# Performance work log

Hardware: AMD Instinct MI355X
Metric: run time of the kernel (lower is better)

Reference implementation:

```python
import jax, jax.numpy as jnp
import numpy as np

E = 1024      # embed_dim (== embed_dim_)
NH = 8        # num_heads
HD = E // NH  # head_dim
BS1 = 2048
BS2 = 2048
EPS = 1e-5


def _layernorm(x, g, b):
    m = jnp.mean(x, axis=-1, keepdims=True)
    v = jnp.mean(jnp.square(x - m), axis=-1, keepdims=True)
    return (x - m) * jax.lax.rsqrt(v + EPS) * g + b


def setup_inputs() -> dict:
    key = jax.random.key(0)
    ks = jax.random.split(key, 16)
    s = 1.0 / np.sqrt(E)
    s4 = 1.0 / np.sqrt(4 * E)
    inp = {
        "x1": jax.random.normal(ks[0], (BS1, E), jnp.float32),
        "x2": jax.random.normal(ks[1], (BS2, E), jnp.float32),
        "Wq": jax.random.uniform(ks[2], (E, E), jnp.float32, -s, s),
        "bq": jax.random.uniform(ks[3], (E,), jnp.float32, -s, s),
        "Wk": jax.random.uniform(ks[4], (E, E), jnp.float32, -s, s),
        "bk": jax.random.uniform(ks[5], (E,), jnp.float32, -s, s),
        "Wv": jax.random.uniform(ks[6], (E, E), jnp.float32, -s, s),
        "bv": jax.random.uniform(ks[7], (E,), jnp.float32, -s, s),
        "Wo": jax.random.uniform(ks[8], (E, E), jnp.float32, -s, s),
        "bo": jax.random.uniform(ks[9], (E,), jnp.float32, -s, s),
        "W1": jax.random.uniform(ks[10], (4 * E, E), jnp.float32, -s, s),
        "b1": jax.random.uniform(ks[11], (4 * E,), jnp.float32, -s, s),
        "W2": jax.random.uniform(ks[12], (E, 4 * E), jnp.float32, -s4, s4),
        "b2": jax.random.uniform(ks[13], (E,), jnp.float32, -s4, s4),
        "g1": jnp.ones((E,), jnp.float32),
        "be1": jnp.zeros((E,), jnp.float32),
        "g2": jnp.ones((E,), jnp.float32),
        "be2": jnp.zeros((E,), jnp.float32),
    }
    return inp


def reference(x1, x2, Wq, bq, Wk, bk, Wv, bv, Wo, bo, W1, b1, W2, b2, g1, be1, g2, be2):
    scale = HD ** -0.5
    # Projections; attention runs over the batch axis (n=bs1, m=bs2)
    q = (x1 @ Wq.T + bq).reshape(BS1, NH, HD)   # [n,h,d]
    k = (x2 @ Wk.T + bk).reshape(BS2, NH, HD)   # [m,h,d]
    v = (x2 @ Wv.T + bv).reshape(BS2, NH, HD)   # [m,h,d]
    scores = jnp.einsum('nhd,mhd->nmh', q, k) * scale  # [n,m,h]
    # NOTE: faithful to source: softmax over the HEADS axis (dim=-1)
    probs = jax.nn.softmax(scores, axis=-1)
    # dropout is identity in eval mode
    attn = jnp.einsum('nmh,mhd->nhd', probs, v).reshape(BS1, E)
    attn = attn @ Wo.T + bo
    h = _layernorm(x1 + attn, g1, be1)
    ffn = jax.nn.relu(h @ W1.T + b1) @ W2.T + b2
    return _layernorm(h + ffn, g2, be2)
```

## Files before the change

kernel.cpp:

```cpp
#include <hip/hip_runtime.h>

#define BS 2048
#define EMB 1024
#define NHEAD 8
#define HDIM 128

typedef unsigned short u16;
typedef __attribute__((ext_vector_type(8))) short bf16x8;
typedef __attribute__((ext_vector_type(4))) float f32x4;

__device__ __forceinline__ u16 f32_bf16(float f) {
  unsigned u = __float_as_uint(f);
  u += 0x7fffu + ((u >> 16) & 1u);
  return (u16)(u >> 16);
}
__device__ __forceinline__ float bf2f(u16 x) {
  return __uint_as_float((unsigned)x << 16);
}

__device__ __forceinline__ void gld_lds16(const void* g, void* l) {
  __builtin_amdgcn_global_load_lds(
      (const __attribute__((address_space(1))) void*)g,
      (__attribute__((address_space(3))) void*)l, 16, 0, 0);
}

struct CvtArgs { const float* src[8]; };
__global__ __launch_bounds__(256) void cvt_all(CvtArgs a, u16* __restrict__ dst) {
  long i = (long)blockIdx.x * 256 + threadIdx.x;
  int seg = (int)(i >> 18);
  const float* src; long b;
  if (seg < 2)       { src = a.src[0]; b = 0; }
  else if (seg < 4)  { src = a.src[1]; b = 2L << 18; }
  else if (seg == 4) { src = a.src[2]; b = 4L << 18; }
  else if (seg == 5) { src = a.src[3]; b = 5L << 18; }
  else if (seg == 6) { src = a.src[4]; b = 6L << 18; }
  else if (seg == 7) { src = a.src[5]; b = 7L << 18; }
  else if (seg < 12) { src = a.src[6]; b = 8L << 18; }
  else               { src = a.src[7]; b = 12L << 18; }
  float4 v = ((const float4*)src)[i - b];
  ushort4 o;
  o.x = f32_bf16(v.x); o.y = f32_bf16(v.y); o.z = f32_bf16(v.z); o.w = f32_bf16(v.w);
  ((ushort4*)dst)[i] = o;
}

__device__ __forceinline__ void gemm_core(
    const u16* __restrict__ A, const u16* __restrict__ B, void* __restrict__ Cp,
    const float* __restrict__ bias, int K, int lda, int ldb, int ldc,
    long cbase, int mode, int relu, int m0, int n0) {
  __shared__ __align__(16) u16 As[128 * 32];
  __shared__ __align__(16) u16 Bs[128 * 32];
  const int t = threadIdx.x;
  const int lane = t & 63, l15 = lane & 15, quad = lane >> 4;
  const int wv = t >> 6, wr = wv & 1, wc = wv >> 1;
  const int wbase = t & ~63;

  f32x4 acc[4][4];
#pragma unroll
  for (int r = 0; r < 4; ++r)
#pragma unroll
    for (int c = 0; c < 4; ++c) acc[r][c] = (f32x4){0.f, 0.f, 0.f, 0.f};

  for (int k0 = 0; k0 < K; k0 += 32) {
#pragma unroll
    for (int i = 0; i < 2; ++i) {
      int s = i * 256 + t;
      gld_lds16(A + (long)(m0 + (s >> 2)) * lda + k0 + (s & 3) * 8,
                As + (i * 256 + wbase) * 8);
    }
#pragma unroll
    for (int i = 0; i < 2; ++i) {
      int s = i * 256 + t;
      gld_lds16(B + (long)(n0 + (s >> 2)) * ldb + k0 + (s & 3) * 8,
                Bs + (i * 256 + wbase) * 8);
    }
    __syncthreads();
    bf16x8 fa[4], fb[4];
#pragma unroll
    for (int r = 0; r < 4; ++r)
      fa[r] = *(const bf16x8*)&As[(wr * 64 + r * 16 + l15) * 32 + quad * 8];
#pragma unroll
    for (int c = 0; c < 4; ++c)
      fb[c] = *(const bf16x8*)&Bs[(wc * 64 + c * 16 + l15) * 32 + quad * 8];
#pragma unroll
    for (int r = 0; r < 4; ++r)
#pragma unroll
      for (int c = 0; c < 4; ++c)
        acc[r][c] = __builtin_amdgcn_mfma_f32_16x16x32_bf16(fa[r], fb[c], acc[r][c], 0, 0, 0);
    __syncthreads();
  }

#pragma unroll
  for (int r = 0; r < 4; ++r)
#pragma unroll
    for (int c = 0; c < 4; ++c) {
      const int m = m0 + wr * 64 + r * 16 + quad * 4;
      const int n = n0 + wc * 64 + c * 16 + l15;
      const float bv = bias ? bias[n] : 0.f;
      f32x4 v = acc[r][c];
      if (mode == 2) {
        ushort4 o;
        o.x = f32_bf16(v[0] + bv);
        o.y = f32_bf16(v[1] + bv);
        o.z = f32_bf16(v[2] + bv);
        o.w = f32_bf16(v[3] + bv);
        *(ushort4*)((u16*)Cp + cbase + (long)n * ldc + m) = o;
      } else {
#pragma unroll
        for (int i = 0; i < 4; ++i) {
          float x = v[i] + bv;
          if (relu) x = fmaxf(x, 0.f);
          if (mode == 0)
            ((float*)Cp)[cbase + (long)(m + i) * ldc + n] = x;
          else
            ((u16*)Cp)[cbase + (long)(m + i) * ldc + n] = f32_bf16(x);
        }
      }
    }
}

__global__ __launch_bounds__(256) void gemm_bt_k(
    const u16* __restrict__ A, const u16* __restrict__ B, void* __restrict__ C,
    const float* __restrict__ bias, int K, int lda, int ldb, int ldc,
    long aOffZ, long bOffZ, long cOffZ, int mode, int relu) {
  gemm_core(A + (long)blockIdx.z * aOffZ, B + (long)blockIdx.z * bOffZ, C, bias,
            K, lda, ldb, ldc, (long)blockIdx.z * cOffZ, mode, relu,
            blockIdx.y * 128, blockIdx.x * 128);
}

__global__ __launch_bounds__(256) void qkv_kernel(
    const u16* __restrict__ x1b, const u16* __restrict__ x2b,
    const u16* __restrict__ Wqb, const u16* __restrict__ Wkb, const u16* __restrict__ Wvb,
    const float* __restrict__ bq, const float* __restrict__ bk, const float* __restrict__ bv,
    u16* __restrict__ Qb, u16* __restrict__ Kb, u16* __restrict__ Vt) {
  const int z = blockIdx.z;
  const u16* A = (z == 0) ? x1b : x2b;
  const u16* B = (z == 0) ? Wqb : (z == 1) ? Wkb : Wvb;
  void* C = (z == 0) ? (void*)Qb : (z == 1) ? (void*)Kb : (void*)Vt;
  const float* bias = (z == 0) ? bq : (z == 1) ? bk : bv;
  const int mode = (z == 2) ? 2 : 1;
  const int ldc = (z == 2) ? 2048 : 1024;
  gemm_core(A, B, C, bias, 1024, 1024, 1024, ldc, 0, mode, 0,
            blockIdx.y * 128, blockIdx.x * 128);
}

__global__ __launch_bounds__(256) void pv_kernel(
    const u16* __restrict__ P, const u16* __restrict__ Vt, u16* __restrict__ parts) {
  const int h = blockIdx.z >> 1, ks = blockIdx.z & 1;
  const u16* A = P + (long)h * BS * BS + ks * 1024;
  const u16* B = Vt + (long)h * HDIM * 2048 + ks * 1024;
  const long cbase = (long)ks * BS * 1024 + h * HDIM;
  gemm_core(A, B, parts, nullptr, 1024, 2048, 2048, 1024, cbase, 1, 0,
            blockIdx.y * 128, 0);
}

__global__ __launch_bounds__(256) void reduce2_bf16(
    const u16* __restrict__ p0, const u16* __restrict__ p1, u16* __restrict__ out) {
  int i = blockIdx.x * 256 + threadIdx.x;
  ushort4 a = ((const ushort4*)p0)[i];
  ushort4 b = ((const ushort4*)p1)[i];
  ushort4 o;
  o.x = f32_bf16(bf2f(a.x) + bf2f(b.x));
  o.y = f32_bf16(bf2f(a.y) + bf2f(b.y));
  o.z = f32_bf16(bf2f(a.z) + bf2f(b.z));
  o.w = f32_bf16(bf2f(a.w) + bf2f(b.w));
  ((ushort4*)out)[i] = o;
}

__global__ __launch_bounds__(256) void scores_softmax(
    const u16* __restrict__ Q, const u16* __restrict__ Km, u16* __restrict__ P) {
  __shared__ __align__(16) u16 Qs[32 * 128];
  __shared__ __align__(16) u16 Ks[128 * 128];
  const int t = threadIdx.x;
  const int lane = t & 63, l15 = lane & 15, quad = lane >> 4;
  const int wv = t >> 6;
  const int n0 = blockIdx.y * 32, m0 = blockIdx.x * 128;
  const int wbase = t & ~63;

  f32x4 acc[8][2][2];
#pragma unroll
  for (int h = 0; h < 8; ++h)
#pragma unroll
    for (int r = 0; r < 2; ++r)
#pragma unroll
      for (int c = 0; c < 2; ++c) acc[h][r][c] = (f32x4){0.f, 0.f, 0.f, 0.f};

#pragma unroll
  for (int h = 0; h < 8; ++h) {
#pragma unroll
    for (int i = 0; i < 2; ++i) {
      int s = i * 256 + t;
      gld_lds16(Q + (long)(n0 + ((s >> 2) & 31)) * EMB + h * HDIM + (s >> 7) * 32 + (s & 3) * 8,
                Qs + (i * 256 + wbase) * 8);
    }
#pragma unroll
    for (int i = 0; i < 8; ++i) {
      int s = i * 256 + t;
      gld_lds16(Km + (long)(m0 + ((s >> 2) & 127)) * EMB + h * HDIM + (s >> 9) * 32 + (s & 3) * 8,
                Ks + (i * 256 + wbase) * 8);
    }
    __syncthreads();
#pragma unroll
    for (int kk = 0; kk < 4; ++kk) {
      bf16x8 fa[2], fb[2];
#pragma unroll
      for (int r = 0; r < 2; ++r)
        fa[r] = *(const bf16x8*)&Qs[kk * 1024 + (r * 16 + l15) * 32 + quad * 8];
#pragma unroll
      for (int c = 0; c < 2; ++c)
        fb[c] = *(const bf16x8*)&Ks[kk * 4096 + (wv * 32 + c * 16 + l15) * 32 + quad * 8];
#pragma unroll
      for (int r = 0; r < 2; ++r)
#pragma unroll
        for (int c = 0; c < 2; ++c)
          acc[h][r][c] = __builtin_amdgcn_mfma_f32_16x16x32_bf16(fa[r], fb[c], acc[h][r][c], 0, 0, 0);
    }
    __syncthreads();
  }

  const float scale = 0.08838834764831845f;
#pragma unroll
  for (int r = 0; r < 2; ++r)
#pragma unroll
    for (int c = 0; c < 2; ++c)
#pragma unroll
      for (int i = 0; i < 4; ++i) {
        float mx = acc[0][r][c][i];
#pragma unroll
        for (int h = 1; h < 8; ++h) mx = fmaxf(mx, acc[h][r][c][i]);
        float sum = 0.f;
#pragma unroll
        for (int h = 0; h < 8; ++h) {
          float e = __expf((acc[h][r][c][i] - mx) * scale);
          acc[h][r][c][i] = e;
          sum += e;
        }
        float inv = 1.f / sum;
#pragma unroll
        for (int h = 0; h < 8; ++h) acc[h][r][c][i] *= inv;
      }

#pragma unroll
  for (int h = 0; h < 8; ++h) {
#pragma unroll
    for (int r = 0; r < 2; ++r)
#pragma unroll
      for (int c = 0; c < 2; ++c)
#pragma unroll
        for (int i = 0; i < 4; ++i) {
          int nl = r * 16 + quad * 4 + i;
          int ml = (wv * 32 + c * 16 + l15) ^ (quad << 3);
          Qs[nl * 128 + ml] = f32_bf16(acc[h][r][c][i]);
        }
    __syncthreads();
#pragma unroll
    for (int j = 0; j < 2; ++j) {
      int ch = j * 256 + t;
      int row = ch >> 4;
      int col = (ch & 15) * 8;
      int sw = ((row >> 2) & 3) << 3;
      uint4 val = *(const uint4*)&Qs[row * 128 + (col ^ sw)];
      *(uint4*)&P[(long)h * BS * BS + (long)(n0 + row) * BS + m0 + col] = val;
    }
    __syncthreads();
  }
}

__global__ __launch_bounds__(256) void ln_residual3(
    const float* __restrict__ x, const float* __restrict__ y0, const float* __restrict__ y1,
    const float* __restrict__ colb, const float* __restrict__ g, const float* __restrict__ b,
    float* __restrict__ out32, u16* __restrict__ out16) {
  const int row = blockIdx.x, t = threadIdx.x;
  float4 v = ((const float4*)(x + (long)row * EMB))[t];
  float4 u0 = ((const float4*)(y0 + (long)row * EMB))[t];
  float4 u1 = ((const float4*)(y1 + (long)row * EMB))[t];
  float4 cb = ((const float4*)colb)[t];
  v.x += u0.x + u1.x + cb.x;
  v.y += u0.y + u1.y + cb.y;
  v.z += u0.z + u1.z + cb.z;
  v.w += u0.w + u1.w + cb.w;
  float s = v.x + v.y + v.z + v.w;
  float q = v.x * v.x + v.y * v.y + v.z * v.z + v.w * v.w;
#pragma unroll
  for (int off = 32; off > 0; off >>= 1) {
    s += __shfl_xor(s, off);
    q += __shfl_xor(q, off);
  }
  __shared__ float red[8];
  const int wv = t >> 6, lane = t & 63;
  if (lane == 0) { red[wv] = s; red[4 + wv] = q; }
  __syncthreads();
  s = red[0] + red[1] + red[2] + red[3];
  q = red[4] + red[5] + red[6] + red[7];
  const float mean = s * (1.f / EMB);
  const float var = q * (1.f / EMB) - mean * mean;
  const float rstd = rsqrtf(var + 1e-5f);
  float4 gg = ((const float4*)g)[t];
  float4 bb = ((const float4*)b)[t];
  float4 o;
  o.x = (v.x - mean) * rstd * gg.x + bb.x;
  o.y = (v.y - mean) * rstd * gg.y + bb.y;
  o.z = (v.z - mean) * rstd * gg.z + bb.z;
  o.w = (v.w - mean) * rstd * gg.w + bb.w;
  ((float4*)(out32 + (long)row * EMB))[t] = o;
  if (out16) {
    ushort4 ho;
    ho.x = f32_bf16(o.x); ho.y = f32_bf16(o.y); ho.z = f32_bf16(o.z); ho.w = f32_bf16(o.w);
    ((ushort4*)(out16 + (long)row * EMB))[t] = ho;
  }
}

extern "C" void kernel_launch(void* const* d_in, const int* in_sizes, int n_in,
                              void* d_out, int out_size, void* d_ws, size_t ws_size,
                              hipStream_t stream) {
  const float* x1 = (const float*)d_in[0];
  const float* x2 = (const float*)d_in[1];
  const float* Wq = (const float*)d_in[2];
  const float* bq = (const float*)d_in[3];
  const float* Wk = (const float*)d_in[4];
  const float* bk = (const float*)d_in[5];
  const float* Wv = (const float*)d_in[6];
  const float* bv = (const float*)d_in[7];
  const float* Wo = (const float*)d_in[8];
  const float* bo = (const float*)d_in[9];
  const float* W1 = (const float*)d_in[10];
  const float* b1 = (const float*)d_in[11];
  const float* W2 = (const float*)d_in[12];
  const float* b2 = (const float*)d_in[13];
  const float* g1 = (const float*)d_in[14];
  const float* be1 = (const float*)d_in[15];
  const float* g2 = (const float*)d_in[16];
  const float* be2 = (const float*)d_in[17];

  char* ws = (char*)d_ws;
  const size_t MB = 1ull << 20;
  u16* x1b = (u16*)(ws + 0 * MB);
  u16* x2b = (u16*)(ws + 4 * MB);
  u16* Wqb = (u16*)(ws + 8 * MB);
  u16* Wkb = (u16*)(ws + 10 * MB);
  u16* Wvb = (u16*)(ws + 12 * MB);
  u16* Wob = (u16*)(ws + 14 * MB);
  u16* W1b = (u16*)(ws + 16 * MB);
  u16* W2b = (u16*)(ws + 24 * MB);
  u16* Qb  = (u16*)(ws + 32 * MB);
  u16* Kb  = (u16*)(ws + 36 * MB);
  u16* pvP0 = Qb;
  u16* pvP1 = Kb;
  u16* Vtb = (u16*)(ws + 40 * MB);
  u16* attnb = (u16*)(ws + 44 * MB);
  u16* P   = (u16*)(ws + 48 * MB);
  float* woP0 = (float*)(ws + 48 * MB);
  float* woP1 = (float*)(ws + 56 * MB);
  float* h32  = (float*)(ws + 64 * MB);
  u16*  h16   = (u16*)(ws + 72 * MB);
  u16*  ffn1b = (u16*)(ws + 76 * MB);
  float* f2P0 = woP0;
  float* f2P1 = woP1;

  CvtArgs ca;
  ca.src[0] = x1; ca.src[1] = x2; ca.src[2] = Wq; ca.src[3] = Wk;
  ca.src[4] = Wv; ca.src[5] = Wo; ca.src[6] = W1; ca.src[7] = W2;
  cvt_all<<<16384, 256, 0, stream>>>(ca, (u16*)ws);

  qkv_kernel<<<dim3(8, 16, 3), 256, 0, stream>>>(x1b, x2b, Wqb, Wkb, Wvb, bq, bk, bv, Qb, Kb, Vtb);

  scores_softmax<<<dim3(16, 64, 1), 256, 0, stream>>>(Qb, Kb, P);

  pv_kernel<<<dim3(1, 16, 16), 256, 0, stream>>>(P, Vtb, pvP0);

  reduce2_bf16<<<2048, 256, 0, stream>>>(pvP0, pvP1, attnb);

  gemm_bt_k<<<dim3(8, 16, 2), 256, 0, stream>>>(attnb, Wob, woP0, nullptr,
                                                512, 1024, 1024, 1024,
                                                512, 512, (long)BS * 1024, 0, 0);

  ln_residual3<<<2048, 256, 0, stream>>>(x1, woP0, woP1, bo, g1, be1, h32, h16);

  gemm_bt_k<<<dim3(32, 16, 1), 256, 0, stream>>>(h16, W1b, ffn1b, b1,
                                                 1024, 1024, 1024, 4096,
                                                 0, 0, 0, 1, 1);

  gemm_bt_k<<<dim3(8, 16, 2), 256, 0, stream>>>(ffn1b, W2b, f2P0, nullptr,
                                                2048, 4096, 4096, 1024,
                                                2048, 2048, (long)BS * 1024, 0, 0);

  ln_residual3<<<2048, 256, 0, stream>>>(h32, f2P0, f2P1, b2, g2, be2, (float*)d_out, nullptr);
}
```

Baseline: 352.1 us.

## Fuse fp32-to-bf16 conversion into GEMM loads and double-buffer score kernel

Removes the separate conversion kernel and has GEMMs read fp32 inputs and weights directly, converting to bf16 while staging into LDS. This avoids writing and re-reading a bf16 copy of all inputs and weights, but the fp32 path uses synchronous register loads in place of direct global-to-LDS loads, and weights are re-converted by every tile. The scores/softmax kernel also double-buffers the per-head Q/K tiles so the next head's loads overlap compute. Its output now goes as scattered 2-byte stores to P rather than through an LDS transpose with coalesced 16-byte writes.

```diff
diff --git a/kernel.cpp b/kernel.cpp
--- a/kernel.cpp
+++ b/kernel.cpp
@@ -24,27 +24,9 @@
       (__attribute__((address_space(3))) void*)l, 16, 0, 0);
 }
 
-struct CvtArgs { const float* src[8]; };
-__global__ __launch_bounds__(256) void cvt_all(CvtArgs a, u16* __restrict__ dst) {
-  long i = (long)blockIdx.x * 256 + threadIdx.x;
-  int seg = (int)(i >> 18);
-  const float* src; long b;
-  if (seg < 2)       { src = a.src[0]; b = 0; }
-  else if (seg < 4)  { src = a.src[1]; b = 2L << 18; }
-  else if (seg == 4) { src = a.src[2]; b = 4L << 18; }
-  else if (seg == 5) { src = a.src[3]; b = 5L << 18; }
-  else if (seg == 6) { src = a.src[4]; b = 6L << 18; }
-  else if (seg == 7) { src = a.src[5]; b = 7L << 18; }
-  else if (seg < 12) { src = a.src[6]; b = 8L << 18; }
-  else               { src = a.src[7]; b = 12L << 18; }
-  float4 v = ((const float4*)src)[i - b];
-  ushort4 o;
-  o.x = f32_bf16(v.x); o.y = f32_bf16(v.y); o.z = f32_bf16(v.z); o.w = f32_bf16(v.w);
-  ((ushort4*)dst)[i] = o;
-}
-
+template <int AF32, int BF32>
 __device__ __forceinline__ void gemm_core(
-    const u16* __restrict__ A, const u16* __restrict__ B, void* __restrict__ Cp,
+    const void* __restrict__ Ap, const void* __restrict__ Bp, void* __restrict__ Cp,
     const float* __restrict__ bias, int K, int lda, int ldb, int ldc,
     long cbase, int mode, int relu, int m0, int n0) {
   __shared__ __align__(16) u16 As[128 * 32];
@@ -64,14 +46,40 @@
 #pragma unroll
     for (int i = 0; i < 2; ++i) {
       int s = i * 256 + t;
-      gld_lds16(A + (long)(m0 + (s >> 2)) * lda + k0 + (s & 3) * 8,
-                As + (i * 256 + wbase) * 8);
+      int row = s >> 2, kc = (s & 3) * 8;
+      if constexpr (AF32) {
+        const float* src = (const float*)Ap + (long)(m0 + row) * lda + k0 + kc;
+        float4 v0 = *(const float4*)src;
+        float4 v1 = *(const float4*)(src + 4);
+        uint4 w;
+        w.x = (unsigned)f32_bf16(v0.x) | ((unsigned)f32_bf16(v0.y) << 16);
+        w.y = (unsigned)f32_bf16(v0.z) | ((unsigned)f32_bf16(v0.w) << 16);
+        w.z = (unsigned)f32_bf16(v1.x) | ((unsigned)f32_bf16(v1.y) << 16);
+        w.w = (unsigned)f32_bf16(v1.z) | ((unsigned)f32_bf16(v1.w) << 16);
+        *(uint4*)&As[row * 32 + kc] = w;
+      } else {
+        gld_lds16((const u16*)Ap + (long)(m0 + row) * lda + k0 + kc,
+                  As + (i * 256 + wbase) * 8);
+      }
     }
 #pragma unroll
     for (int i = 0; i < 2; ++i) {
       int s = i * 256 + t;
-      gld_lds16(B + (long)(n0 + (s >> 2)) * ldb + k0 + (s & 3) * 8,
-                Bs + (i * 256 + wbase) * 8);
+      int row = s >> 2, kc = (s & 3) * 8;
+      if constexpr (BF32) {
+        const float* src = (const float*)Bp + (long)(n0 + row) * ldb + k0 + kc;
+        float4 v0 = *(const float4*)src;
+        float4 v1 = *(const float4*)(src + 4);
+        uint4 w;
+        w.x = (unsigned)f32_bf16(v0.x) | ((unsigned)f32_bf16(v0.y) << 16);
+        w.y = (unsigned)f32_bf16(v0.z) | ((unsigned)f32_bf16(v0.w) << 16);
+        w.z = (unsigned)f32_bf16(v1.x) | ((unsigned)f32_bf16(v1.y) << 16);
+        w.w = (unsigned)f32_bf16(v1.z) | ((unsigned)f32_bf16(v1.w) << 16);
+        *(uint4*)&Bs[row * 32 + kc] = w;
+      } else {
+        gld_lds16((const u16*)Bp + (long)(n0 + row) * ldb + k0 + kc,
+                  Bs + (i * 256 + wbase) * 8);
+      }
     }
     __syncthreads();
     bf16x8 fa[4], fb[4];
@@ -118,29 +126,34 @@
     }
 }
 
+template <int AF32, int BF32>
 __global__ __launch_bounds__(256) void gemm_bt_k(
-    const u16* __restrict__ A, const u16* __restrict__ B, void* __restrict__ C,
+    const void* __restrict__ A, const void* __restrict__ B, void* __restrict__ C,
     const float* __restrict__ bias, int K, int lda, int ldb, int ldc,
     long aOffZ, long bOffZ, long cOffZ, int mode, int relu) {
-  gemm_core(A + (long)blockIdx.z * aOffZ, B + (long)blockIdx.z * bOffZ, C, bias,
-            K, lda, ldb, ldc, (long)blockIdx.z * cOffZ, mode, relu,
-            blockIdx.y * 128, blockIdx.x * 128);
+  const void* Az = AF32 ? (const void*)((const float*)A + (long)blockIdx.z * aOffZ)
+                        : (const void*)((const u16*)A + (long)blockIdx.z * aOffZ);
+  const void* Bz = BF32 ? (const void*)((const float*)B + (long)blockIdx.z * bOffZ)
+                        : (const void*)((const u16*)B + (long)blockIdx.z * bOffZ);
+  gemm_core<AF32, BF32>(Az, Bz, C, bias, K, lda, ldb, ldc,
+                        (long)blockIdx.z * cOffZ, mode, relu,
+                        blockIdx.y * 128, blockIdx.x * 128);
 }
 
 __global__ __launch_bounds__(256) void qkv_kernel(
-    const u16* __restrict__ x1b, const u16* __restrict__ x2b,
-    const u16* __restrict__ Wqb, const u16* __restrict__ Wkb, const u16* __restrict__ Wvb,
+    const float* __restrict__ x1, const float* __restrict__ x2,
+    const float* __restrict__ Wq, const float* __restrict__ Wk, const float* __restrict__ Wv,
     const float* __restrict__ bq, const float* __restrict__ bk, const float* __restrict__ bv,
     u16* __restrict__ Qb, u16* __restrict__ Kb, u16* __restrict__ Vt) {
   const int z = blockIdx.z;
-  const u16* A = (z == 0) ? x1b : x2b;
-  const u16* B = (z == 0) ? Wqb : (z == 1) ? Wkb : Wvb;
+  const float* A = (z == 0) ? x1 : x2;
+  const float* B = (z == 0) ? Wq : (z == 1) ? Wk : Wv;
   void* C = (z == 0) ? (void*)Qb : (z == 1) ? (void*)Kb : (void*)Vt;
   const float* bias = (z == 0) ? bq : (z == 1) ? bk : bv;
   const int mode = (z == 2) ? 2 : 1;
   const int ldc = (z == 2) ? 2048 : 1024;
-  gemm_core(A, B, C, bias, 1024, 1024, 1024, ldc, 0, mode, 0,
-            blockIdx.y * 128, blockIdx.x * 128);
+  gemm_core<1, 1>(A, B, C, bias, 1024, 1024, 1024, ldc, 0, mode, 0,
+                  blockIdx.y * 128, blockIdx.x * 128);
 }
 
 __global__ __launch_bounds__(256) void pv_kernel(
@@ -149,8 +162,8 @@
   const u16* A = P + (long)h * BS * BS + ks * 1024;
   const u16* B = Vt + (long)h * HDIM * 2048 + ks * 1024;
   const long cbase = (long)ks * BS * 1024 + h * HDIM;
-  gemm_core(A, B, parts, nullptr, 1024, 2048, 2048, 1024, cbase, 1, 0,
-            blockIdx.y * 128, 0);
+  gemm_core<0, 0>(A, B, parts, nullptr, 1024, 2048, 2048, 1024, cbase, 1, 0,
+                  blockIdx.y * 128, 0);
 }
 
 __global__ __launch_bounds__(256) void reduce2_bf16(
@@ -168,53 +181,58 @@
 
 __global__ __launch_bounds__(256) void scores_softmax(
     const u16* __restrict__ Q, const u16* __restrict__ Km, u16* __restrict__ P) {
-  __shared__ __align__(16) u16 Qs[32 * 128];
-  __shared__ __align__(16) u16 Ks[128 * 128];
+  __shared__ __align__(16) u16 Qs[2][4096];
+  __shared__ __align__(16) u16 Ks[2][16384];
   const int t = threadIdx.x;
   const int lane = t & 63, l15 = lane & 15, quad = lane >> 4;
-  const int wv = t >> 6;
+  const int wv = t >> 6, wbase = t & ~63;
   const int n0 = blockIdx.y * 32, m0 = blockIdx.x * 128;
-  const int wbase = t & ~63;
-
-  f32x4 acc[8][2][2];
-#pragma unroll
-  for (int h = 0; h < 8; ++h)
-#pragma unroll
-    for (int r = 0; r < 2; ++r)
-#pragma unroll
-      for (int c = 0; c < 2; ++c) acc[h][r][c] = (f32x4){0.f, 0.f, 0.f, 0.f};
-
-#pragma unroll
-  for (int h = 0; h < 8; ++h) {
+
+  auto stage = [&](int h, int b) {
 #pragma unroll
     for (int i = 0; i < 2; ++i) {
       int s = i * 256 + t;
       gld_lds16(Q + (long)(n0 + ((s >> 2) & 31)) * EMB + h * HDIM + (s >> 7) * 32 + (s & 3) * 8,
-                Qs + (i * 256 + wbase) * 8);
+                &Qs[b][(i * 256 + wbase) * 8]);
     }
 #pragma unroll
     for (int i = 0; i < 8; ++i) {
       int s = i * 256 + t;
       gld_lds16(Km + (long)(m0 + ((s >> 2) & 127)) * EMB + h * HDIM + (s >> 9) * 32 + (s & 3) * 8,
-                Ks + (i * 256 + wbase) * 8);
-    }
+                &Ks[b][(i * 256 + wbase) * 8]);
+    }
+  };
+
+  f32x4 acc[8][2][2];
+#pragma unroll
+  for (int h = 0; h < 8; ++h)
+#pragma unroll
+    for (int r = 0; r < 2; ++r)
+#pragma unroll
+      for (int c = 0; c < 2; ++c) acc[h][r][c] = (f32x4){0.f, 0.f, 0.f, 0.f};
+
+  stage(0, 0);
+#pragma unroll
+  for (int h = 0; h < 8; ++h) {
     __syncthreads();
+    if (h < 7) stage(h + 1, (h + 1) & 1);
+    const u16* qb = Qs[h & 1];
+    const u16* kb = Ks[h & 1];
 #pragma unroll
     for (int kk = 0; kk < 4; ++kk) {
       bf16x8 fa[2], fb[2];
 #pragma unroll
       for (int r = 0; r < 2; ++r)
-        fa[r] = *(const bf16x8*)&Qs[kk * 1024 + (r * 16 + l15) * 32 + quad * 8];
+        fa[r] = *(const bf16x8*)&qb[kk * 1024 + (r * 16 + l15) * 32 + quad * 8];
 #pragma unroll
       for (int c = 0; c < 2; ++c)
-        fb[c] = *(const bf16x8*)&Ks[kk * 4096 + (wv * 32 + c * 16 + l15) * 32 + quad * 8];
+        fb[c] = *(const bf16x8*)&kb[kk * 4096 + (wv * 32 + c * 16 + l15) * 32 + quad * 8];
 #pragma unroll
       for (int r = 0; r < 2; ++r)
 #pragma unroll
         for (int c = 0; c < 2; ++c)
           acc[h][r][c] = __builtin_amdgcn_mfma_f32_16x16x32_bf16(fa[r], fb[c], acc[h][r][c], 0, 0, 0);
     }
-    __syncthreads();
   }
 
   const float scale = 0.08838834764831845f;
@@ -241,27 +259,15 @@
 
 #pragma unroll
   for (int h = 0; h < 8; ++h) {
+    u16* ph = P + (long)h * BS * BS;
 #pragma unroll
     for (int r = 0; r < 2; ++r)
 #pragma unroll
       for (int c = 0; c < 2; ++c)
 #pragma unroll
-        for (int i = 0; i < 4; ++i) {
-          int nl = r * 16 + quad * 4 + i;
-          int ml = (wv * 32 + c * 16 + l15) ^ (quad << 3);
-          Qs[nl * 128 + ml] = f32_bf16(acc[h][r][c][i]);
-        }
-    __syncthreads();
-#pragma unroll
-    for (int j = 0; j < 2; ++j) {
-      int ch = j * 256 + t;
-      int row = ch >> 4;
-      int col = (ch & 15) * 8;
-      int sw = ((row >> 2) & 3) << 3;
-      uint4 val = *(const uint4*)&Qs[row * 128 + (col ^ sw)];
-      *(uint4*)&P[(long)h * BS * BS + (long)(n0 + row) * BS + m0 + col] = val;
-    }
-    __syncthreads();
+        for (int i = 0; i < 4; ++i)
+          ph[(long)(n0 + r * 16 + quad * 4 + i) * BS + m0 + wv * 32 + c * 16 + l15] =
+              f32_bf16(acc[h][r][c][i]);
   }
 }
 
@@ -333,55 +339,41 @@
 
   char* ws = (char*)d_ws;
   const size_t MB = 1ull << 20;
-  u16* x1b = (u16*)(ws + 0 * MB);
-  u16* x2b = (u16*)(ws + 4 * MB);
-  u16* Wqb = (u16*)(ws + 8 * MB);
-  u16* Wkb = (u16*)(ws + 10 * MB);
-  u16* Wvb = (u16*)(ws + 12 * MB);
-  u16* Wob = (u16*)(ws + 14 * MB);
-  u16* W1b = (u16*)(ws + 16 * MB);
-  u16* W2b = (u16*)(ws + 24 * MB);
-  u16* Qb  = (u16*)(ws + 32 * MB);
-  u16* Kb  = (u16*)(ws + 36 * MB);
-  u16* pvP0 = Qb;
-  u16* pvP1 = Kb;
-  u16* Vtb = (u16*)(ws + 40 * MB);
-  u16* attnb = (u16*)(ws + 44 * MB);
-  u16* P   = (u16*)(ws + 48 * MB);
-  float* woP0 = (float*)(ws + 48 * MB);
-  float* woP1 = (float*)(ws + 56 * MB);
-  float* h32  = (float*)(ws + 64 * MB);
-  u16*  h16   = (u16*)(ws + 72 * MB);
-  u16*  ffn1b = (u16*)(ws + 76 * MB);
+  u16* Qb  = (u16*)(ws + 0 * MB);
+  u16* Kb  = (u16*)(ws + 4 * MB);
+  u16* Vtb = (u16*)(ws + 8 * MB);
+  u16* attnb = (u16*)(ws + 12 * MB);
+  u16* P   = (u16*)(ws + 16 * MB);
+  u16* pvParts = Qb;
+  float* woP0 = (float*)(ws + 16 * MB);
+  float* woP1 = (float*)(ws + 24 * MB);
+  float* h32  = (float*)(ws + 32 * MB);
+  u16*  h16   = (u16*)(ws + 40 * MB);
+  u16*  ffn1b = (u16*)(ws + 44 * MB);
   float* f2P0 = woP0;
   float* f2P1 = woP1;
 
-  CvtArgs ca;
-  ca.src[0] = x1; ca.src[1] = x2; ca.src[2] = Wq; ca.src[3] = Wk;
-  ca.src[4] = Wv; ca.src[5] = Wo; ca.src[6] = W1; ca.src[7] = W2;
-  cvt_all<<<16384, 256, 0, stream>>>(ca, (u16*)ws);
-
-  qkv_kernel<<<dim3(8, 16, 3), 256, 0, stream>>>(x1b, x2b, Wqb, Wkb, Wvb, bq, bk, bv, Qb, Kb, Vtb);
-
-  scores_softmax<<<dim3(16, 64, 1), 256, 0, stream>>>(Qb, Kb, P);
-
-  pv_kernel<<<dim3(1, 16, 16), 256, 0, stream>>>(P, Vtb, pvP0);
-
-  reduce2_bf16<<<2048, 256, 0, stream>>>(pvP0, pvP1, attnb);
-
-  gemm_bt_k<<<dim3(8, 16, 2), 256, 0, stream>>>(attnb, Wob, woP0, nullptr,
-                                                512, 1024, 1024, 1024,
-                                                512, 512, (long)BS * 1024, 0, 0);
+  qkv_kernel<<<dim3(8, 16, 3), 256, 0, stream>>>(x1, x2, Wq, Wk, Wv, bq, bk, bv, Qb, Kb, Vtb);
+
+  scores_softmax<<<dim3(16, 64), 256, 0, stream>>>(Qb, Kb, P);
+
+  pv_kernel<<<dim3(1, 16, 16), 256, 0, stream>>>(P, Vtb, pvParts);
+
+  reduce2_bf16<<<2048, 256, 0, stream>>>(pvParts, pvParts + (long)BS * EMB, attnb);
+
+  gemm_bt_k<0, 1><<<dim3(8, 16, 2), 256, 0, stream>>>(attnb, Wo, woP0, nullptr,
+                                                      512, 1024, 1024, 1024,
+                                                      512, 512, (long)BS * 1024, 0, 0);
 
   ln_residual3<<<2048, 256, 0, stream>>>(x1, woP0, woP1, bo, g1, be1, h32, h16);
 
-  gemm_bt_k<<<dim3(32, 16, 1), 256, 0, stream>>>(h16, W1b, ffn1b, b1,
-                                                 1024, 1024, 1024, 4096,
-                                                 0, 0, 0, 1, 1);
-
-  gemm_bt_k<<<dim3(8, 16, 2), 256, 0, stream>>>(ffn1b, W2b, f2P0, nullptr,
-                                                2048, 4096, 4096, 1024,
-                                                2048, 2048, (long)BS * 1024, 0, 0);
+  gemm_bt_k<0, 1><<<dim3(32, 16, 1), 256, 0, stream>>>(h16, W1, ffn1b, b1,
+                                                       1024, 1024, 1024, 4096,
+                                                       0, 0, 0, 1, 1);
+
+  gemm_bt_k<0, 1><<<dim3(8, 16, 2), 256, 0, stream>>>(ffn1b, W2, f2P0, nullptr,
+                                                      2048, 4096, 4096, 1024,
+                                                      2048, 2048, (long)BS * 1024, 0, 0);
 
   ln_residual3<<<2048, 256, 0, stream>>>(h32, f2P0, f2P1, b2, g2, be2, (float*)d_out, nullptr);
 }
```

Measured after the change: 421.0 us. +19.6%, slower.

## Raise split-K to four, double-buffer score staging, store bf16 partials directly

Applied to the files above, without the earlier changes.

The PV, Wo and FFN2 GEMMs move from split-K 2 to split-K 4, which doubles the grid size for better occupancy. The Wo and FFN2 partials are now written as bf16 instead of fp32, and the LayerNorm kernels sum the four partials. The scores kernel double-buffers the per-head Q/K LDS staging so the next head's loads overlap the current head's MFMAs. It also drops the LDS-transposed P store in favour of direct scattered global stores. Costs: more partial traffic, extra bf16 rounding error, and less coalesced P writes.

```diff
diff --git a/kernel.cpp b/kernel.cpp
--- a/kernel.cpp
+++ b/kernel.cpp
@@ -144,77 +144,86 @@
 }
 
 __global__ __launch_bounds__(256) void pv_kernel(
-    const u16* __restrict__ P, const u16* __restrict__ Vt, u16* __restrict__ parts) {
-  const int h = blockIdx.z >> 1, ks = blockIdx.z & 1;
-  const u16* A = P + (long)h * BS * BS + ks * 1024;
-  const u16* B = Vt + (long)h * HDIM * 2048 + ks * 1024;
-  const long cbase = (long)ks * BS * 1024 + h * HDIM;
-  gemm_core(A, B, parts, nullptr, 1024, 2048, 2048, 1024, cbase, 1, 0,
+    const u16* __restrict__ P, const u16* __restrict__ Vt,
+    u16* p0, u16* p1, u16* p2, u16* p3) {
+  const int h = blockIdx.z >> 2, ks = blockIdx.z & 3;
+  u16* parts = (ks == 0) ? p0 : (ks == 1) ? p1 : (ks == 2) ? p2 : p3;
+  const u16* A = P + (long)h * BS * BS + ks * 512;
+  const u16* B = Vt + (long)h * HDIM * 2048 + ks * 512;
+  gemm_core(A, B, parts, nullptr, 512, 2048, 2048, 1024, (long)h * HDIM, 1, 0,
             blockIdx.y * 128, 0);
 }
 
-__global__ __launch_bounds__(256) void reduce2_bf16(
-    const u16* __restrict__ p0, const u16* __restrict__ p1, u16* __restrict__ out) {
-  int i = blockIdx.x * 256 + threadIdx.x;
+__global__ __launch_bounds__(256) void reduce4p_bf16(
+    const u16* __restrict__ p0, const u16* __restrict__ p1,
+    const u16* __restrict__ p2, const u16* __restrict__ p3, u16* __restrict__ out) {
+  long i = (long)blockIdx.x * 256 + threadIdx.x;
   ushort4 a = ((const ushort4*)p0)[i];
   ushort4 b = ((const ushort4*)p1)[i];
+  ushort4 c = ((const ushort4*)p2)[i];
+  ushort4 d = ((const ushort4*)p3)[i];
   ushort4 o;
-  o.x = f32_bf16(bf2f(a.x) + bf2f(b.x));
-  o.y = f32_bf16(bf2f(a.y) + bf2f(b.y));
-  o.z = f32_bf16(bf2f(a.z) + bf2f(b.z));
-  o.w = f32_bf16(bf2f(a.w) + bf2f(b.w));
+  o.x = f32_bf16(bf2f(a.x) + bf2f(b.x) + bf2f(c.x) + bf2f(d.x));
+  o.y = f32_bf16(bf2f(a.y) + bf2f(b.y) + bf2f(c.y) + bf2f(d.y));
+  o.z = f32_bf16(bf2f(a.z) + bf2f(b.z) + bf2f(c.z) + bf2f(d.z));
+  o.w = f32_bf16(bf2f(a.w) + bf2f(b.w) + bf2f(c.w) + bf2f(d.w));
   ((ushort4*)out)[i] = o;
 }
 
 __global__ __launch_bounds__(256) void scores_softmax(
     const u16* __restrict__ Q, const u16* __restrict__ Km, u16* __restrict__ P) {
-  __shared__ __align__(16) u16 Qs[32 * 128];
-  __shared__ __align__(16) u16 Ks[128 * 128];
+  __shared__ __align__(16) u16 Qs[2][4096];
+  __shared__ __align__(16) u16 Ks[2][16384];
   const int t = threadIdx.x;
   const int lane = t & 63, l15 = lane & 15, quad = lane >> 4;
-  const int wv = t >> 6;
+  const int wv = t >> 6, wbase = t & ~63;
   const int n0 = blockIdx.y * 32, m0 = blockIdx.x * 128;
-  const int wbase = t & ~63;
-
-  f32x4 acc[8][2][2];
-#pragma unroll
-  for (int h = 0; h < 8; ++h)
-#pragma unroll
-    for (int r = 0; r < 2; ++r)
-#pragma unroll
-      for (int c = 0; c < 2; ++c) acc[h][r][c] = (f32x4){0.f, 0.f, 0.f, 0.f};
-
-#pragma unroll
-  for (int h = 0; h < 8; ++h) {
+
+  auto stage = [&](int h, int b) {
 #pragma unroll
     for (int i = 0; i < 2; ++i) {
       int s = i * 256 + t;
       gld_lds16(Q + (long)(n0 + ((s >> 2) & 31)) * EMB + h * HDIM + (s >> 7) * 32 + (s & 3) * 8,
-                Qs + (i * 256 + wbase) * 8);
+                &Qs[b][(i * 256 + wbase) * 8]);
     }
 #pragma unroll
     for (int i = 0; i < 8; ++i) {
       int s = i * 256 + t;
       gld_lds16(Km + (long)(m0 + ((s >> 2) & 127)) * EMB + h * HDIM + (s >> 9) * 32 + (s & 3) * 8,
-                Ks + (i * 256 + wbase) * 8);
-    }
+                &Ks[b][(i * 256 + wbase) * 8]);
+    }
+  };
+
+  f32x4 acc[8][2][2];
+#pragma unroll
+  for (int h = 0; h < 8; ++h)
+#pragma unroll
+    for (int r = 0; r < 2; ++r)
+#pragma unroll
+      for (int c = 0; c < 2; ++c) acc[h][r][c] = (f32x4){0.f, 0.f, 0.f, 0.f};
+
+  stage(0, 0);
+#pragma unroll
+  for (int h = 0; h < 8; ++h) {
     __syncthreads();
+    if (h < 7) stage(h + 1, (h + 1) & 1);
+    const u16* qb = Qs[h & 1];
+    const u16* kb = Ks[h & 1];
 #pragma unroll
     for (int kk = 0; kk < 4; ++kk) {
       bf16x8 fa[2], fb[2];
 #pragma unroll
       for (int r = 0; r < 2; ++r)
-        fa[r] = *(const bf16x8*)&Qs[kk * 1024 + (r * 16 + l15) * 32 + quad * 8];
+        fa[r] = *(const bf16x8*)&qb[kk * 1024 + (r * 16 + l15) * 32 + quad * 8];
 #pragma unroll
       for (int c = 0; c < 2; ++c)
-        fb[c] = *(const bf16x8*)&Ks[kk * 4096 + (wv * 32 + c * 16 + l15) * 32 + quad * 8];
+        fb[c] = *(const bf16x8*)&kb[kk * 4096 + (wv * 32 + c * 16 + l15) * 32 + quad * 8];
 #pragma unroll
       for (int r = 0; r < 2; ++r)
 #pragma unroll
         for (int c = 0; c < 2; ++c)
           acc[h][r][c] = __builtin_amdgcn_mfma_f32_16x16x32_bf16(fa[r], fb[c], acc[h][r][c], 0, 0, 0);
     }
-    __syncthreads();
   }
 
   const float scale = 0.08838834764831845f;
@@ -241,43 +250,36 @@
 
 #pragma unroll
   for (int h = 0; h < 8; ++h) {
+    u16* ph = P + (long)h * BS * BS;
 #pragma unroll
     for (int r = 0; r < 2; ++r)
 #pragma unroll
       for (int c = 0; c < 2; ++c)
 #pragma unroll
-        for (int i = 0; i < 4; ++i) {
-          int nl = r * 16 + quad * 4 + i;
-          int ml = (wv * 32 + c * 16 + l15) ^ (quad << 3);
-          Qs[nl * 128 + ml] = f32_bf16(acc[h][r][c][i]);
-        }
-    __syncthreads();
-#pragma unroll
-    for (int j = 0; j < 2; ++j) {
-      int ch = j * 256 + t;
-      int row = ch >> 4;
-      int col = (ch & 15) * 8;
-      int sw = ((row >> 2) & 3) << 3;
-      uint4 val = *(const uint4*)&Qs[row * 128 + (col ^ sw)];
-      *(uint4*)&P[(long)h * BS * BS + (long)(n0 + row) * BS + m0 + col] = val;
-    }
-    __syncthreads();
-  }
-}
-
-__global__ __launch_bounds__(256) void ln_residual3(
-    const float* __restrict__ x, const float* __restrict__ y0, const float* __restrict__ y1,
+        for (int i = 0; i < 4; ++i)
+          ph[(long)(n0 + r * 16 + quad * 4 + i) * BS + m0 + wv * 32 + c * 16 + l15] =
+              f32_bf16(acc[h][r][c][i]);
+  }
+}
+
+__global__ __launch_bounds__(256) void ln_residual_p4(
+    const float* __restrict__ x,
+    const u16* __restrict__ p0, const u16* __restrict__ p1,
+    const u16* __restrict__ p2, const u16* __restrict__ p3,
     const float* __restrict__ colb, const float* __restrict__ g, const float* __restrict__ b,
     float* __restrict__ out32, u16* __restrict__ out16) {
   const int row = blockIdx.x, t = threadIdx.x;
-  float4 v = ((const float4*)(x + (long)row * EMB))[t];
-  float4 u0 = ((const float4*)(y0 + (long)row * EMB))[t];
-  float4 u1 = ((const float4*)(y1 + (long)row * EMB))[t];
+  const long base = (long)row * EMB;
+  float4 v = ((const float4*)(x + base))[t];
+  ushort4 a0 = ((const ushort4*)(p0 + base))[t];
+  ushort4 a1 = ((const ushort4*)(p1 + base))[t];
+  ushort4 a2 = ((const ushort4*)(p2 + base))[t];
+  ushort4 a3 = ((const ushort4*)(p3 + base))[t];
   float4 cb = ((const float4*)colb)[t];
-  v.x += u0.x + u1.x + cb.x;
-  v.y += u0.y + u1.y + cb.y;
-  v.z += u0.z + u1.z + cb.z;
-  v.w += u0.w + u1.w + cb.w;
+  v.x += bf2f(a0.x) + bf2f(a1.x) + bf2f(a2.x) + bf2f(a3.x) + cb.x;
+  v.y += bf2f(a0.y) + bf2f(a1.y) + bf2f(a2.y) + bf2f(a3.y) + cb.y;
+  v.z += bf2f(a0.z) + bf2f(a1.z) + bf2f(a2.z) + bf2f(a3.z) + cb.z;
+  v.w += bf2f(a0.w) + bf2f(a1.w) + bf2f(a2.w) + bf2f(a3.w) + cb.w;
   float s = v.x + v.y + v.z + v.w;
   float q = v.x * v.x + v.y * v.y + v.z * v.z + v.w * v.w;
 #pragma unroll
@@ -301,11 +303,11 @@
   o.y = (v.y - mean) * rstd * gg.y + bb.y;
   o.z = (v.z - mean) * rstd * gg.z + bb.z;
   o.w = (v.w - mean) * rstd * gg.w + bb.w;
-  ((float4*)(out32 + (long)row * EMB))[t] = o;
+  ((float4*)(out32 + base))[t] = o;
   if (out16) {
     ushort4 ho;
     ho.x = f32_bf16(o.x); ho.y = f32_bf16(o.y); ho.z = f32_bf16(o.z); ho.w = f32_bf16(o.w);
-    ((ushort4*)(out16 + (long)row * EMB))[t] = ho;
+    ((ushort4*)(out16 + base))[t] = ho;
   }
 }
 
@@ -343,18 +345,16 @@
   u16* W2b = (u16*)(ws + 24 * MB);
   u16* Qb  = (u16*)(ws + 32 * MB);
   u16* Kb  = (u16*)(ws + 36 * MB);
-  u16* pvP0 = Qb;
-  u16* pvP1 = Kb;
   u16* Vtb = (u16*)(ws + 40 * MB);
   u16* attnb = (u16*)(ws + 44 * MB);
   u16* P   = (u16*)(ws + 48 * MB);
-  float* woP0 = (float*)(ws + 48 * MB);
-  float* woP1 = (float*)(ws + 56 * MB);
+  u16* woP[4] = {(u16*)(ws + 48 * MB), (u16*)(ws + 52 * MB),
+                 (u16*)(ws + 56 * MB), (u16*)(ws + 60 * MB)};
   float* h32  = (float*)(ws + 64 * MB);
   u16*  h16   = (u16*)(ws + 72 * MB);
   u16*  ffn1b = (u16*)(ws + 76 * MB);
-  float* f2P0 = woP0;
-  float* f2P1 = woP1;
+  u16* f2P[4] = {(u16*)(ws + 92 * MB), (u16*)(ws + 96 * MB),
+                 (u16*)(ws + 100 * MB), (u16*)(ws + 104 * MB)};
 
   CvtArgs ca;
   ca.src[0] = x1; ca.src[1] = x2; ca.src[2] = Wq; ca.src[3] = Wk;
@@ -363,25 +363,27 @@
 
   qkv_kernel<<<dim3(8, 16, 3), 256, 0, stream>>>(x1b, x2b, Wqb, Wkb, Wvb, bq, bk, bv, Qb, Kb, Vtb);
 
-  scores_softmax<<<dim3(16, 64, 1), 256, 0, stream>>>(Qb, Kb, P);
-
-  pv_kernel<<<dim3(1, 16, 16), 256, 0, stream>>>(P, Vtb, pvP0);
-
-  reduce2_bf16<<<2048, 256, 0, stream>>>(pvP0, pvP1, attnb);
-
-  gemm_bt_k<<<dim3(8, 16, 2), 256, 0, stream>>>(attnb, Wob, woP0, nullptr,
-                                                512, 1024, 1024, 1024,
-                                                512, 512, (long)BS * 1024, 0, 0);
-
-  ln_residual3<<<2048, 256, 0, stream>>>(x1, woP0, woP1, bo, g1, be1, h32, h16);
+  scores_softmax<<<dim3(16, 64), 256, 0, stream>>>(Qb, Kb, P);
+
+  pv_kernel<<<dim3(1, 16, 32), 256, 0, stream>>>(P, Vtb, x1b, x2b, Qb, Kb);
+
+  reduce4p_bf16<<<2048, 256, 0, stream>>>(x1b, x2b, Qb, Kb, attnb);
+
+  gemm_bt_k<<<dim3(8, 16, 4), 256, 0, stream>>>(attnb, Wob, woP[0], nullptr,
+                                                256, 1024, 1024, 1024,
+                                                256, 256, (long)BS * 1024, 1, 0);
+
+  ln_residual_p4<<<2048, 256, 0, stream>>>(x1, woP[0], woP[1], woP[2], woP[3],
+                                           bo, g1, be1, h32, h16);
 
   gemm_bt_k<<<dim3(32, 16, 1), 256, 0, stream>>>(h16, W1b, ffn1b, b1,
                                                  1024, 1024, 1024, 4096,
                                                  0, 0, 0, 1, 1);
 
-  gemm_bt_k<<<dim3(8, 16, 2), 256, 0, stream>>>(ffn1b, W2b, f2P0, nullptr,
-                                                2048, 4096, 4096, 1024,
-                                                2048, 2048, (long)BS * 1024, 0, 0);
-
-  ln_residual3<<<2048, 256, 0, stream>>>(h32, f2P0, f2P1, b2, g2, be2, (float*)d_out, nullptr);
-}
+  gemm_bt_k<<<dim3(8, 16, 4), 256, 0, stream>>>(ffn1b, W2b, f2P[0], nullptr,
+                                                1024, 4096, 4096, 1024,
+                                                1024, 1024, (long)BS * 1024, 1, 0);
+
+  ln_residual_p4<<<2048, 256, 0, stream>>>(h32, f2P[0], f2P[1], f2P[2], f2P[3],
+                                           b2, g2, be2, (float*)d_out, nullptr);
+}
```

Result: faster. 339.2 us (-3.6%).
